# Kernel tuning notes

Measured on AMD Instinct MI355X. Metric: run time of the kernel, lower is better.

## Reference

```python
import jax, jax.numpy as jnp
import numpy as np

N, D_IN, D_OUT = 4096, 1024, 1024
DROPOUT_RATE = 0.1


def setup_inputs() -> dict:
    key = jax.random.key(0)
    kx, kq, kk, kv = jax.random.split(key, 4)
    s = 1.0 / np.sqrt(D_IN)
    return {
        "x": jax.random.normal(kx, (N, D_IN), dtype=jnp.float32),
        "wq": jax.random.normal(kq, (D_OUT, D_IN), dtype=jnp.float32) * s,
        "wk": jax.random.normal(kk, (D_OUT, D_IN), dtype=jnp.float32) * s,
        "wv": jax.random.normal(kv, (D_OUT, D_IN), dtype=jnp.float32) * s,
    }


def reference(x, wq, wk, wv):
    # torch Linear: y = x @ W.T  (no bias since qkv_bias=False)
    q = x @ wq.T                      # [N, d_out]
    k = x @ wk.T
    v = x @ wv.T
    scores = q @ k.T                  # [N, N]
    n = scores.shape[0]
    causal = jnp.tril(jnp.ones((n, n), dtype=bool))  # keep lower triangle
    masked = jnp.where(causal, scores, -jnp.inf)
    scale = k.shape[-1] ** 0.5
    weights = jax.nn.softmax(masked / scale, axis=-1)
    # dropout (train mode), fixed key for determinism
    keep = jax.random.bernoulli(jax.random.key(42), 1.0 - DROPOUT_RATE, weights.shape)
    weights = jnp.where(keep, weights / (1.0 - DROPOUT_RATE), 0.0)
    return weights @ v                # [N, d_out]
```

## Files before the change

kernel.cpp:

```cpp
#include <hip/hip_runtime.h>
#include <hip/hip_fp16.h>

typedef __attribute__((ext_vector_type(8))) _Float16 f16x8;
typedef __attribute__((ext_vector_type(4))) float f32x4;

typedef const __attribute__((address_space(1))) void gas_void;
typedef __attribute__((address_space(3))) void las_void;
typedef __attribute__((address_space(3))) const __half las_chalf;

__device__ __forceinline__ f16x8 ldsr(const __half* p) {
    f16x8 r;
    asm volatile("ds_read_b128 %0, %1" : "=v"(r) : "v"((las_chalf*)p));
    return r;
}

__global__ __launch_bounds__(256) void cast_all_k(const float* __restrict__ x,
                                                  const float* __restrict__ wq,
                                                  const float* __restrict__ wk,
                                                  const float* __restrict__ wv,
                                                  __half* __restrict__ xb,
                                                  __half* __restrict__ wqkv) {
    const int b = blockIdx.x;
    const float* src;
    __half* dst;
    size_t i;
    if (b < 2048) {
        src = x; dst = xb;
        i = ((size_t)b * 256 + threadIdx.x) * 8;
    } else {
        const int w = (b - 2048) >> 9;
        src = w == 0 ? wq : (w == 1 ? wk : wv);
        dst = wqkv + (size_t)w * 1048576;
        i = (((size_t)((b - 2048) & 511)) * 256 + threadIdx.x) * 8;
    }
    float4 a = *(const float4*)(src + i);
    float4 c = *(const float4*)(src + i + 4);
    __half2 h[4] = { __floats2half2_rn(a.x, a.y), __floats2half2_rn(a.z, a.w),
                     __floats2half2_rn(c.x, c.y), __floats2half2_rn(c.z, c.w) };
    *(int4*)(dst + i) = *(int4*)h;
}

__global__ __launch_bounds__(256) void transpose_f16_k(const __half* __restrict__ in,
                                                       __half* __restrict__ out,
                                                       int R, int ldin) {
    __shared__ __half t[64][72];
    int r0 = blockIdx.x * 64, c0 = blockIdx.y * 64;
    for (int idx = threadIdx.x; idx < 64 * 64; idx += 256) {
        int r = idx >> 6, c = idx & 63;
        t[r][c] = in[(size_t)(r0 + r) * ldin + c0 + c];
    }
    __syncthreads();
    for (int idx = threadIdx.x; idx < 64 * 64; idx += 256) {
        int r = idx >> 6, c = idx & 63;
        out[(size_t)(c0 + r) * R + r0 + c] = t[c][r];
    }
}

__device__ __forceinline__ void storeC(__half* C, size_t off, float v) { C[off] = __float2half(v); }
__device__ __forceinline__ void storeC(float*  C, size_t off, float v) { C[off] = v; }

template <typename CT, bool LOWER_ONLY, bool SPLITK>
__global__ __launch_bounds__(512, 2)
void gemm256(const __half* __restrict__ A, const __half* __restrict__ B, CT* __restrict__ C,
             float* __restrict__ P1, float* __restrict__ P2, float* __restrict__ P3,
             int lda, int ldb, int ldc, int NTin, float scale) {
    int bi, c = 0;
    const int bj = blockIdx.y;
    if (SPLITK) {
        int x = blockIdx.x;
        if (x < 4)       { bi = x;                    c = 0; }
        else if (x < 12) { bi = 4  + ((x - 4) >> 1);  c = (x - 4) & 1; }
        else if (x < 24) { bi = 8  + (x - 12) / 3;    c = (x - 12) % 3; }
        else             { bi = 12 + ((x - 24) >> 2); c = (x - 24) & 3; }
    } else {
        bi = blockIdx.x;
        if (LOWER_ONLY && bj > bi) return;
    }
    const int brow = bi * 256, bcol = bj * 256;
    const int tid = threadIdx.x;
    const int lane = tid & 63, wid = tid >> 6;
    const int wm = wid >> 2, wn = wid & 3;
    const int lane15 = lane & 15;
    const int kxor = (lane & 7) << 3;
    const int g16 = (lane >> 4) << 3;

    int k_lo = 0, NT = NTin;
    if (SPLITK) { int full = 4 * (bi + 1); k_lo = c * 16; NT = min(full - k_lo, 16); }

    extern __shared__ __half smem[];

    const int srow = (wid << 3) + (lane >> 3);
    const int scol = ((lane & 7) ^ ((lane >> 3) & 7)) << 3;

    auto stage_half = [&](const __half* G, int ldg, int growbase, int kt, int buf, int mat, int half) {
        const __half* src = G + (size_t)(growbase + half * 128 + srow) * ldg + kt * 64 + scol;
        __half* dst = &smem[buf * 32768 + mat * 16384 + (half * 128 + (wid << 3)) * 64];
        __builtin_amdgcn_global_load_lds((gas_void*)src, (las_void*)dst, 16, 0, 0);
        __builtin_amdgcn_global_load_lds((gas_void*)(src + (size_t)64 * ldg),
                                         (las_void*)(dst + 64 * 64), 16, 0, 0);
    };

    f32x4 acc[8][4] = {};
    f16x8 bfrag[2][4];

    stage_half(B, ldb, bcol, k_lo, 0, 1, 0);
    stage_half(B, ldb, bcol, k_lo, 0, 1, 1);
    stage_half(A, lda, brow, k_lo, 0, 0, 0);
    stage_half(A, lda, brow, k_lo, 0, 0, 1);
    if (NT > 1) {
        stage_half(B, ldb, bcol, k_lo + 1, 1, 1, 0);
        stage_half(B, ldb, bcol, k_lo + 1, 1, 1, 1);
    }

    for (int Tr = 0; Tr < NT; ++Tr) {
        const int Ta = k_lo + Tr;
        const int buf = Tr & 1;
        const __half* Abase = &smem[buf * 32768 + (wm * 128 + lane15) * 64];
        const __half* Bbase = &smem[buf * 32768 + 16384 + (wn * 64 + lane15) * 64];

        if (Tr < NT - 1) asm volatile("s_waitcnt vmcnt(4)" ::: "memory");
        else             asm volatile("s_waitcnt vmcnt(0)" ::: "memory");
        __builtin_amdgcn_s_barrier();

        {
#pragma unroll
            for (int kk = 0; kk < 2; ++kk)
#pragma unroll
                for (int n = 0; n < 4; ++n)
                    bfrag[kk][n] = ldsr(Bbase + (n * 16) * 64 + ((kk * 32 + g16) ^ kxor));
            f16x8 af[2][2];
#pragma unroll
            for (int mi = 0; mi < 2; ++mi)
#pragma unroll
                for (int kk = 0; kk < 2; ++kk)
                    af[mi][kk] = ldsr(Abase + (mi * 16) * 64 + ((kk * 32 + g16) ^ kxor));
            if (Tr + 1 < NT) stage_half(A, lda, brow, Ta + 1, buf ^ 1, 0, 0);
            asm volatile("s_waitcnt lgkmcnt(0)" ::: "memory");
            __builtin_amdgcn_sched_barrier(0);
            __builtin_amdgcn_s_setprio(1);
#pragma unroll
            for (int mi = 0; mi < 2; ++mi)
#pragma unroll
                for (int n = 0; n < 4; ++n)
#pragma unroll
                    for (int kk = 0; kk < 2; ++kk)
                        acc[mi][n] = __builtin_amdgcn_mfma_f32_16x16x32_f16(
                            af[mi][kk], bfrag[kk][n], acc[mi][n], 0, 0, 0);
            __builtin_amdgcn_s_setprio(0);
            __builtin_amdgcn_s_barrier();
        }

#pragma unroll
        for (int p = 1; p < 4; ++p) {
            f16x8 af[2][2];
#pragma unroll
            for (int mi = 0; mi < 2; ++mi)
#pragma unroll
                for (int kk = 0; kk < 2; ++kk)
                    af[mi][kk] = ldsr(Abase + ((2 * p + mi) * 16) * 64 + ((kk * 32 + g16) ^ kxor));
            if (p == 1)      { if (Tr + 1 < NT) stage_half(A, lda, brow, Ta + 1, buf ^ 1, 0, 1); }
            else if (p == 2) { if (Tr + 2 < NT) stage_half(B, ldb, bcol, Ta + 2, buf, 1, 0); }
            else             { if (Tr + 2 < NT) stage_half(B, ldb, bcol, Ta + 2, buf, 1, 1); }
            asm volatile("s_waitcnt lgkmcnt(0)" ::: "memory");
            __builtin_amdgcn_sched_barrier(0);
            __builtin_amdgcn_s_setprio(1);
#pragma unroll
            for (int mi = 0; mi < 2; ++mi)
#pragma unroll
                for (int n = 0; n < 4; ++n)
#pragma unroll
                    for (int kk = 0; kk < 2; ++kk)
                        acc[2 * p + mi][n] = __builtin_amdgcn_mfma_f32_16x16x32_f16(
                            af[mi][kk], bfrag[kk][n], acc[2 * p + mi][n], 0, 0, 0);
            __builtin_amdgcn_s_setprio(0);
            __builtin_amdgcn_s_barrier();
        }
    }

    CT* Ct = C;
    if (SPLITK && c > 0) Ct = (CT*)(c == 1 ? P1 : (c == 2 ? P2 : P3));
    const int r0 = (lane >> 4) << 2;
#pragma unroll
    for (int m = 0; m < 8; ++m) {
#pragma unroll
        for (int n = 0; n < 4; ++n) {
            int col = bcol + wn * 64 + n * 16 + lane15;
#pragma unroll
            for (int r = 0; r < 4; ++r) {
                int row = brow + wm * 128 + m * 16 + r0 + r;
                storeC(Ct, (size_t)row * ldc + col, acc[m][n][r] * scale);
            }
        }
    }
}

__global__ __launch_bounds__(256) void pv_scale_reduce_k(float* __restrict__ out,
                                                         const float* __restrict__ P1,
                                                         const float* __restrict__ P2,
                                                         const float* __restrict__ P3,
                                                         const float* __restrict__ L) {
    const int row = blockIdx.x;
    const float inv = 1.0f / (0.9f * L[row]);
    const size_t o = (size_t)row * 1024 + threadIdx.x * 4;
    float4 s = *(float4*)(out + o);
    if (row >= 1024) {
        float4 a = *(const float4*)(P1 + o);
        s.x += a.x; s.y += a.y; s.z += a.z; s.w += a.w;
    }
    if (row >= 2048) {
        float4 b = *(const float4*)(P2 + o);
        s.x += b.x; s.y += b.y; s.z += b.z; s.w += b.w;
    }
    if (row >= 3072) {
        float4 d = *(const float4*)(P3 + o);
        s.x += d.x; s.y += d.y; s.z += d.z; s.w += d.w;
    }
    s.x *= inv; s.y *= inv; s.z *= inv; s.w *= inv;
    *(float4*)(out + o) = s;
}

__device__ __forceinline__ uint32_t rotl32(uint32_t x, int d) { return (x << d) | (x >> (32 - d)); }

__device__ __forceinline__ bool keep_bit(uint32_t flat) {
    uint32_t x0 = 0u;
    uint32_t x1 = flat;
    const uint32_t ks0 = 0u, ks1 = 42u, ks2 = 0u ^ 42u ^ 0x1BD11BDAu;
    x0 += ks0; x1 += ks1;
#define TFR(r) { x0 += x1; x1 = rotl32(x1, r); x1 ^= x0; }
    TFR(13) TFR(15) TFR(26) TFR(6)   x0 += ks1; x1 += ks2 + 1u;
    TFR(17) TFR(29) TFR(16) TFR(24)  x0 += ks2; x1 += ks0 + 2u;
    TFR(13) TFR(15) TFR(26) TFR(6)   x0 += ks0; x1 += ks1 + 3u;
    TFR(17) TFR(29) TFR(16) TFR(24)  x0 += ks1; x1 += ks2 + 4u;
    TFR(13) TFR(15) TFR(26) TFR(6)   x0 += ks2; x1 += ks0 + 5u;
#undef TFR
    uint32_t bits = x0 ^ x1;
    float u = __uint_as_float((bits >> 9) | 0x3f800000u) - 1.0f;
    return u < 0.9f;
}

__global__ __launch_bounds__(256) void softdrop_k(__half* __restrict__ SP,
                                                  float* __restrict__ L, int N) {
    const int i = blockIdx.x;
    const int tid = threadIdx.x;
    const int len = i + 1;
    __half* row = SP + (size_t)i * N;

    float l = 0.f;
    const int len8 = len & ~7;
    for (int j = tid * 8; j < len8; j += 2048) {
        int4 pk = *(const int4*)(row + j);
        const __half* hp = (const __half*)&pk;
        __half o8[8];
        const uint32_t base = (uint32_t)i * 4096u + (uint32_t)j;
#pragma unroll
        for (int q = 0; q < 8; ++q) {
            float e = __expf(__half2float(hp[q]));
            l += e;
            o8[q] = keep_bit(base + q) ? __float2half(e) : __float2half(0.0f);
        }
        *(int4*)(row + j) = *(int4*)o8;
    }
    for (int j = len8 + tid; j < len; j += 256) {
        float e = __expf(__half2float(row[j]));
        l += e;
        row[j] = keep_bit((uint32_t)i * 4096u + (uint32_t)j) ? __float2half(e) : __float2half(0.0f);
    }

    for (int off = 1; off < 64; off <<= 1) l += __shfl_xor(l, off);
    __shared__ float ls[4];
    if ((tid & 63) == 0) ls[tid >> 6] = l;
    __syncthreads();
    if (tid == 0) L[i] = ls[0] + ls[1] + ls[2] + ls[3];

    const int zlim = ((i >> 8) << 8) + 256;
    const int za = (len + 7) & ~7;
    for (int j = len + tid; j < min(za, zlim); j += 256) row[j] = __float2half(0.0f);
    const int4 z = {0, 0, 0, 0};
    for (int j = za + tid * 8; j < zlim; j += 2048) *(int4*)(row + j) = z;
}

extern "C" void kernel_launch(void* const* d_in, const int* in_sizes, int n_in,
                              void* d_out, int out_size, void* d_ws, size_t ws_size,
                              hipStream_t stream) {
    const float* x  = (const float*)d_in[0];
    const float* wq = (const float*)d_in[1];
    const float* wk = (const float*)d_in[2];
    const float* wv = (const float*)d_in[3];
    float* out = (float*)d_out;
    char* ws = (char*)d_ws;

    const int N = 4096, D = 1024;

    __half* xb   = (__half*)(ws + 0);
    __half* wqkv = (__half*)(ws + 8388608);
    __half* QKV  = (__half*)(ws + 14680064);
    __half* VT   = (__half*)(ws + 39845888);
    __half* SP   = (__half*)(ws + 48234496);
    float*  Lr   = (float*)(ws + 81788928);

    float* P1 = (float*)(ws + 14680064) - (size_t)1024 * 1024;
    float* P2 = (float*)(ws + 14680064 + 12582912) - (size_t)2048 * 1024;
    float* P3 = (float*)(ws + 14680064 + 20971520) - (size_t)3072 * 1024;

    __half* Q = QKV;
    __half* K = QKV + 1024;
    __half* V = QKV + 2048;

    auto* gqkv_f = gemm256<__half, false, false>;
    auto* gs_f   = gemm256<__half, true,  false>;
    auto* gpv_f  = gemm256<float,  false, true>;
    (void)hipFuncSetAttribute((const void*)gqkv_f, hipFuncAttributeMaxDynamicSharedMemorySize, 131072);
    (void)hipFuncSetAttribute((const void*)gs_f,   hipFuncAttributeMaxDynamicSharedMemorySize, 131072);
    (void)hipFuncSetAttribute((const void*)gpv_f,  hipFuncAttributeMaxDynamicSharedMemorySize, 131072);

    cast_all_k<<<3584, 256, 0, stream>>>(x, wq, wk, wv, xb, wqkv);

    dim3 gq(N / 256, 3 * D / 256);
    gqkv_f<<<gq, 512, 131072, stream>>>(xb, wqkv, QKV, nullptr, nullptr, nullptr,
                                        D, D, 3 * D, D / 64, 1.0f);

    dim3 gt(N / 64, D / 64);
    transpose_f16_k<<<gt, 256, 0, stream>>>(V, VT, N, 3 * D);

    dim3 gsd(N / 256, N / 256);
    gs_f<<<gsd, 512, 131072, stream>>>(Q, K, SP, nullptr, nullptr, nullptr,
                                       3 * D, 3 * D, N, D / 64, 0.03125f);

    softdrop_k<<<N, 256, 0, stream>>>(SP, Lr, N);

    dim3 go(40, D / 256);
    gpv_f<<<go, 512, 131072, stream>>>(SP, VT, out, P1, P2, P3,
                                       N, N, D, 0, 1.0f);

    pv_scale_reduce_k<<<N, 256, 0, stream>>>(out, P1, P2, P3, Lr);
}
```

Measured before the change: 151.6 us.

## Compute V transposed in QKV GEMM, compact causal grid, fold scaling into PV epilogue

The QKV projection kernel now also computes V^T directly as Wv·X^T, so the separate transpose kernel is dropped. The QK^T GEMM launches only lower-triangle tiles through a triangular index map instead of early-exiting blocks. All three GEMMs use a 1D grid with an XCD-aware swizzle and compile-time leading dimensions. The PV GEMM applies the 1/(0.9·L) normalisation in its epilogue for the first 1024 rows, so the reduce kernel only handles the remaining 3072 rows. The price is a more complex index mapping and reshuffled workspace offsets for the split-K partial buffers.

```diff
diff --git a/kernel.cpp b/kernel.cpp
--- a/kernel.cpp
+++ b/kernel.cpp
@@ -40,42 +40,50 @@
     *(int4*)(dst + i) = *(int4*)h;
 }
 
-__global__ __launch_bounds__(256) void transpose_f16_k(const __half* __restrict__ in,
-                                                       __half* __restrict__ out,
-                                                       int R, int ldin) {
-    __shared__ __half t[64][72];
-    int r0 = blockIdx.x * 64, c0 = blockIdx.y * 64;
-    for (int idx = threadIdx.x; idx < 64 * 64; idx += 256) {
-        int r = idx >> 6, c = idx & 63;
-        t[r][c] = in[(size_t)(r0 + r) * ldin + c0 + c];
-    }
-    __syncthreads();
-    for (int idx = threadIdx.x; idx < 64 * 64; idx += 256) {
-        int r = idx >> 6, c = idx & 63;
-        out[(size_t)(c0 + r) * R + r0 + c] = t[c][r];
-    }
-}
-
-__device__ __forceinline__ void storeC(__half* C, size_t off, float v) { C[off] = __float2half(v); }
-__device__ __forceinline__ void storeC(float*  C, size_t off, float v) { C[off] = v; }
-
-template <typename CT, bool LOWER_ONLY, bool SPLITK>
+template <int MODE>
 __global__ __launch_bounds__(512, 2)
-void gemm256(const __half* __restrict__ A, const __half* __restrict__ B, CT* __restrict__ C,
+void gemm256(const __half* __restrict__ pA, const __half* __restrict__ pB,
+             void* __restrict__ pC, void* __restrict__ pC2,
              float* __restrict__ P1, float* __restrict__ P2, float* __restrict__ P3,
-             int lda, int ldb, int ldc, int NTin, float scale) {
-    int bi, c = 0;
-    const int bj = blockIdx.y;
-    if (SPLITK) {
-        int x = blockIdx.x;
+             const float* __restrict__ Lr) {
+    constexpr int LDA = (MODE == 0) ? 1024 : (MODE == 1 ? 2048 : 4096);
+    constexpr int LDB = (MODE == 0) ? 1024 : (MODE == 1 ? 2048 : 4096);
+    constexpr float SCALE = (MODE == 1) ? 0.03125f : 1.0f;
+
+    int bi, bj, c = 0, k_lo = 0, NT = 16;
+    bool isVT = false;
+    if constexpr (MODE == 0) {
+        const int id = blockIdx.x;
+        const int sw = (id & 7) * 24 + (id >> 3);
+        if (sw < 128) { bi = sw >> 3; bj = sw & 7; }
+        else          { int s2 = sw - 128; bi = s2 >> 4; bj = s2 & 15; isVT = true; }
+    } else if constexpr (MODE == 1) {
+        const int id = blockIdx.x;
+        const int sw = (id & 7) * 17 + (id >> 3);
+        int b = (int)((sqrtf(8.0f * sw + 1.0f) - 1.0f) * 0.5f);
+        while ((b + 1) * (b + 2) / 2 <= sw) ++b;
+        while (b * (b + 1) / 2 > sw) --b;
+        bi = b; bj = sw - b * (b + 1) / 2;
+    } else {
+        const int id = blockIdx.x;
+        const int sw = (id & 7) * 20 + (id >> 3);
+        bj = sw / 40;
+        const int x = sw - 40 * bj;
         if (x < 4)       { bi = x;                    c = 0; }
         else if (x < 12) { bi = 4  + ((x - 4) >> 1);  c = (x - 4) & 1; }
         else if (x < 24) { bi = 8  + (x - 12) / 3;    c = (x - 12) % 3; }
         else             { bi = 12 + ((x - 24) >> 2); c = (x - 24) & 3; }
-    } else {
-        bi = blockIdx.x;
-        if (LOWER_ONLY && bj > bi) return;
-    }
+        const int full = 4 * (bi + 1);
+        k_lo = c * 16;
+        NT = min(full - k_lo, 16);
+    }
+
+    const __half* A = pA;
+    const __half* B = pB;
+    if constexpr (MODE == 0) {
+        if (isVT) { A = pB + 2097152; B = pA; }
+    }
+
     const int brow = bi * 256, bcol = bj * 256;
     const int tid = threadIdx.x;
     const int lane = tid & 63, wid = tid >> 6;
@@ -84,9 +92,6 @@
     const int kxor = (lane & 7) << 3;
     const int g16 = (lane >> 4) << 3;
 
-    int k_lo = 0, NT = NTin;
-    if (SPLITK) { int full = 4 * (bi + 1); k_lo = c * 16; NT = min(full - k_lo, 16); }
-
     extern __shared__ __half smem[];
 
     const int srow = (wid << 3) + (lane >> 3);
@@ -103,13 +108,13 @@
     f32x4 acc[8][4] = {};
     f16x8 bfrag[2][4];
 
-    stage_half(B, ldb, bcol, k_lo, 0, 1, 0);
-    stage_half(B, ldb, bcol, k_lo, 0, 1, 1);
-    stage_half(A, lda, brow, k_lo, 0, 0, 0);
-    stage_half(A, lda, brow, k_lo, 0, 0, 1);
+    stage_half(B, LDB, bcol, k_lo, 0, 1, 0);
+    stage_half(B, LDB, bcol, k_lo, 0, 1, 1);
+    stage_half(A, LDA, brow, k_lo, 0, 0, 0);
+    stage_half(A, LDA, brow, k_lo, 0, 0, 1);
     if (NT > 1) {
-        stage_half(B, ldb, bcol, k_lo + 1, 1, 1, 0);
-        stage_half(B, ldb, bcol, k_lo + 1, 1, 1, 1);
+        stage_half(B, LDB, bcol, k_lo + 1, 1, 1, 0);
+        stage_half(B, LDB, bcol, k_lo + 1, 1, 1, 1);
     }
 
     for (int Tr = 0; Tr < NT; ++Tr) {
@@ -134,7 +139,7 @@
 #pragma unroll
                 for (int kk = 0; kk < 2; ++kk)
                     af[mi][kk] = ldsr(Abase + (mi * 16) * 64 + ((kk * 32 + g16) ^ kxor));
-            if (Tr + 1 < NT) stage_half(A, lda, brow, Ta + 1, buf ^ 1, 0, 0);
+            if (Tr + 1 < NT) stage_half(A, LDA, brow, Ta + 1, buf ^ 1, 0, 0);
             asm volatile("s_waitcnt lgkmcnt(0)" ::: "memory");
             __builtin_amdgcn_sched_barrier(0);
             __builtin_amdgcn_s_setprio(1);
@@ -158,9 +163,9 @@
 #pragma unroll
                 for (int kk = 0; kk < 2; ++kk)
                     af[mi][kk] = ldsr(Abase + ((2 * p + mi) * 16) * 64 + ((kk * 32 + g16) ^ kxor));
-            if (p == 1)      { if (Tr + 1 < NT) stage_half(A, lda, brow, Ta + 1, buf ^ 1, 0, 1); }
-            else if (p == 2) { if (Tr + 2 < NT) stage_half(B, ldb, bcol, Ta + 2, buf, 1, 0); }
-            else             { if (Tr + 2 < NT) stage_half(B, ldb, bcol, Ta + 2, buf, 1, 1); }
+            if (p == 1)      { if (Tr + 1 < NT) stage_half(A, LDA, brow, Ta + 1, buf ^ 1, 0, 1); }
+            else if (p == 2) { if (Tr + 2 < NT) stage_half(B, LDB, bcol, Ta + 2, buf, 1, 0); }
+            else             { if (Tr + 2 < NT) stage_half(B, LDB, bcol, Ta + 2, buf, 1, 1); }
             asm volatile("s_waitcnt lgkmcnt(0)" ::: "memory");
             __builtin_amdgcn_sched_barrier(0);
             __builtin_amdgcn_s_setprio(1);
@@ -177,18 +182,40 @@
         }
     }
 
-    CT* Ct = C;
-    if (SPLITK && c > 0) Ct = (CT*)(c == 1 ? P1 : (c == 2 ? P2 : P3));
     const int r0 = (lane >> 4) << 2;
-#pragma unroll
-    for (int m = 0; m < 8; ++m) {
-#pragma unroll
-        for (int n = 0; n < 4; ++n) {
-            int col = bcol + wn * 64 + n * 16 + lane15;
+    if constexpr (MODE == 2) {
+        float* Ct = (float*)pC;
+        if (c == 1) Ct = P1; else if (c == 2) Ct = P2; else if (c == 3) Ct = P3;
+        const bool doScale = (c == 0) && (bi < 4);
+#pragma unroll
+        for (int m = 0; m < 8; ++m) {
 #pragma unroll
             for (int r = 0; r < 4; ++r) {
-                int row = brow + wm * 128 + m * 16 + r0 + r;
-                storeC(Ct, (size_t)row * ldc + col, acc[m][n][r] * scale);
+                const int row = brow + wm * 128 + m * 16 + r0 + r;
+                const float inv = doScale ? 1.0f / (0.9f * Lr[row]) : 1.0f;
+#pragma unroll
+                for (int n = 0; n < 4; ++n) {
+                    const int col = bcol + wn * 64 + n * 16 + lane15;
+                    Ct[(size_t)row * 1024 + col] = acc[m][n][r] * inv;
+                }
+            }
+        }
+    } else {
+        __half* Ct = (__half*)pC;
+        int ldc = (MODE == 1) ? 4096 : 2048;
+        if constexpr (MODE == 0) {
+            if (isVT) { Ct = (__half*)pC2; ldc = 4096; }
+        }
+#pragma unroll
+        for (int m = 0; m < 8; ++m) {
+#pragma unroll
+            for (int n = 0; n < 4; ++n) {
+                const int col = bcol + wn * 64 + n * 16 + lane15;
+#pragma unroll
+                for (int r = 0; r < 4; ++r) {
+                    const int row = brow + wm * 128 + m * 16 + r0 + r;
+                    Ct[(size_t)row * ldc + col] = __float2half(acc[m][n][r] * SCALE);
+                }
             }
         }
     }
@@ -199,14 +226,12 @@
                                                          const float* __restrict__ P2,
                                                          const float* __restrict__ P3,
                                                          const float* __restrict__ L) {
-    const int row = blockIdx.x;
+    const int row = 1024 + blockIdx.x;
     const float inv = 1.0f / (0.9f * L[row]);
     const size_t o = (size_t)row * 1024 + threadIdx.x * 4;
     float4 s = *(float4*)(out + o);
-    if (row >= 1024) {
-        float4 a = *(const float4*)(P1 + o);
-        s.x += a.x; s.y += a.y; s.z += a.z; s.w += a.w;
-    }
+    float4 a = *(const float4*)(P1 + o);
+    s.x += a.x; s.y += a.y; s.z += a.z; s.w += a.w;
     if (row >= 2048) {
         float4 b = *(const float4*)(P2 + o);
         s.x += b.x; s.y += b.y; s.z += b.z; s.w += b.w;
@@ -293,44 +318,34 @@
 
     __half* xb   = (__half*)(ws + 0);
     __half* wqkv = (__half*)(ws + 8388608);
-    __half* QKV  = (__half*)(ws + 14680064);
-    __half* VT   = (__half*)(ws + 39845888);
+    __half* QK   = (__half*)(ws + 14680064);
+    __half* VT   = (__half*)(ws + 31457280);
     __half* SP   = (__half*)(ws + 48234496);
     float*  Lr   = (float*)(ws + 81788928);
 
     float* P1 = (float*)(ws + 14680064) - (size_t)1024 * 1024;
-    float* P2 = (float*)(ws + 14680064 + 12582912) - (size_t)2048 * 1024;
-    float* P3 = (float*)(ws + 14680064 + 20971520) - (size_t)3072 * 1024;
-
-    __half* Q = QKV;
-    __half* K = QKV + 1024;
-    __half* V = QKV + 2048;
-
-    auto* gqkv_f = gemm256<__half, false, false>;
-    auto* gs_f   = gemm256<__half, true,  false>;
-    auto* gpv_f  = gemm256<float,  false, true>;
-    (void)hipFuncSetAttribute((const void*)gqkv_f, hipFuncAttributeMaxDynamicSharedMemorySize, 131072);
-    (void)hipFuncSetAttribute((const void*)gs_f,   hipFuncAttributeMaxDynamicSharedMemorySize, 131072);
-    (void)hipFuncSetAttribute((const void*)gpv_f,  hipFuncAttributeMaxDynamicSharedMemorySize, 131072);
+    float* P3 = (float*)(ws + 27262976) - (size_t)3072 * 1024;
+    float* P2 = (float*)(ws + 39845888) - (size_t)2048 * 1024;
+
+    __half* Q = QK;
+    __half* K = QK + 1024;
+
+    auto* g0 = gemm256<0>;
+    auto* g1 = gemm256<1>;
+    auto* g2 = gemm256<2>;
+    (void)hipFuncSetAttribute((const void*)g0, hipFuncAttributeMaxDynamicSharedMemorySize, 131072);
+    (void)hipFuncSetAttribute((const void*)g1, hipFuncAttributeMaxDynamicSharedMemorySize, 131072);
+    (void)hipFuncSetAttribute((const void*)g2, hipFuncAttributeMaxDynamicSharedMemorySize, 131072);
 
     cast_all_k<<<3584, 256, 0, stream>>>(x, wq, wk, wv, xb, wqkv);
 
-    dim3 gq(N / 256, 3 * D / 256);
-    gqkv_f<<<gq, 512, 131072, stream>>>(xb, wqkv, QKV, nullptr, nullptr, nullptr,
-                                        D, D, 3 * D, D / 64, 1.0f);
-
-    dim3 gt(N / 64, D / 64);
-    transpose_f16_k<<<gt, 256, 0, stream>>>(V, VT, N, 3 * D);
-
-    dim3 gsd(N / 256, N / 256);
-    gs_f<<<gsd, 512, 131072, stream>>>(Q, K, SP, nullptr, nullptr, nullptr,
-                                       3 * D, 3 * D, N, D / 64, 0.03125f);
+    g0<<<192, 512, 131072, stream>>>(xb, wqkv, QK, VT, nullptr, nullptr, nullptr, nullptr);
+
+    g1<<<136, 512, 131072, stream>>>(Q, K, SP, nullptr, nullptr, nullptr, nullptr, nullptr);
 
     softdrop_k<<<N, 256, 0, stream>>>(SP, Lr, N);
 
-    dim3 go(40, D / 256);
-    gpv_f<<<go, 512, 131072, stream>>>(SP, VT, out, P1, P2, P3,
-                                       N, N, D, 0, 1.0f);
-
-    pv_scale_reduce_k<<<N, 256, 0, stream>>>(out, P1, P2, P3, Lr);
-}
+    g2<<<160, 512, 131072, stream>>>(SP, VT, out, nullptr, P1, P2, P3, Lr);
+
+    pv_scale_reduce_k<<<3072, 256, 0, stream>>>(out, P1, P2, P3, Lr);
+}
```

Result: faster. 145.5 us (-4.0%).
